# Optimization experiments

Measured on AMD Instinct MI355X. Metric: run time of the kernel, lower is better.

## Reference

```python
import jax, jax.numpy as jnp
import numpy as np

N = 50000      # nodes
E = 1600000    # edges (avg degree 32)
IN = 128       # input feature dim
H = 4          # heads
C = 16         # out channels per head
NEG_SLOPE = 0.2


def setup_inputs() -> dict:
    key = jax.random.key(0)
    k = jax.random.split(key, 6)
    x = jax.random.normal(k[0], (N, IN), jnp.float32)
    edge_index = jax.random.randint(k[1], (2, E), 0, N, dtype=jnp.int32).astype(jnp.int64)
    W = jax.random.normal(k[2], (H * C, IN), jnp.float32) * (1.0 / np.sqrt(IN))
    att_src = jax.random.normal(k[3], (H, C), jnp.float32) * 0.1
    att_dst = jax.random.normal(k[4], (H, C), jnp.float32) * 0.1
    bias = jax.random.normal(k[5], (H * C,), jnp.float32) * 0.01
    return {"x": x, "edge_index": edge_index, "W": W,
            "att_src": att_src, "att_dst": att_dst, "bias": bias}


def reference(x, edge_index, W, att_src, att_dst, bias):
    # shared linear projection (PyG GATConv lin, no bias): [N, H, C]
    xp = (x @ W.T).reshape(-1, H, C)
    # per-node attention logits: [N, H]
    a_src = jnp.einsum('nhc,hc->nh', xp, att_src)
    a_dst = jnp.einsum('nhc,hc->nh', xp, att_dst)
    src, dst = edge_index[0], edge_index[1]  # messages flow src(j) -> dst(i)
    # per-edge scores: [E, H]
    e = jax.nn.leaky_relu(a_src[src] + a_dst[dst], negative_slope=NEG_SLOPE)
    # segment softmax over destination neighborhoods
    m = jax.ops.segment_max(e, dst, num_segments=N)           # [N, H]
    m = jnp.where(jnp.isfinite(m), m, 0.0)                     # empty segments
    ex = jnp.exp(e - m[dst])
    s = jax.ops.segment_sum(ex, dst, num_segments=N)           # [N, H]
    alpha = ex / (s[dst] + 1e-16)                              # [E, H]
    # weighted messages, scatter-add to destinations
    msg = (alpha[:, :, None] * xp[src]).reshape(E, H * C)      # [E, H*C]
    out = jax.ops.segment_sum(msg, dst, num_segments=N)        # [N, H*C]
    return out + bias
```

## Files before the change

kernel.cpp:

```cpp
#include <hip/hip_runtime.h>
#include <hip/hip_bf16.h>
#include <math.h>

#define N_NODES 50000
#define N_EDGES 1600000
#define IN_DIM  128
#define HC      64
#define NH      4
#define SLOTS   72
#define BSHIFT  4
#define BNODES  16
#define NB      3125
#define BCAP    768
#define GEMM_BLOCKS 391
#define FAT_GRID 587
#define FAT_LDS 33792

__global__ __launch_bounds__(512) void gemm_bucket_kernel(
    const float* __restrict__ x, const float* __restrict__ W,
    const float* __restrict__ att_src, const float* __restrict__ att_dst,
    const int* __restrict__ ei,
    __hip_bfloat16* __restrict__ xp, float* __restrict__ a_src,
    float* __restrict__ a_dst,
    int* __restrict__ gcursor, unsigned int* __restrict__ barr) {
    extern __shared__ char smraw[];
    int tid = (int)threadIdx.x;
    int bx  = (int)blockIdx.x;
    bool is_bucket = (bx % 3) == 1;

    if (!is_bucket) {
        int gb = bx - (bx + 1) / 3;
        float* Wl = (float*)smraw;
        const float4* W4 = (const float4*)W;
#pragma unroll
        for (int j = 0; j < 4; ++j) {
            int f = j * 512 + tid;
            int c = f >> 5, k4 = f & 31;
            *(float4*)&Wl[c * 132 + k4 * 4] = W4[f];
        }
        __syncthreads();

        int l = tid & 63, w = tid >> 6, q = l >> 4, i = l & 15;
        int n0 = gb * 128 + w * 16 + q * 4;
        int nj[4];
#pragma unroll
        for (int j = 0; j < 4; ++j) {
            int n = n0 + j;
            nj[j] = (n < N_NODES) ? n : N_NODES - 1;
        }
        const float* wlp = Wl + i * 132;
        float4 acc[4] = {{0,0,0,0},{0,0,0,0},{0,0,0,0},{0,0,0,0}};
        float4 xr[4], xn[4];
#pragma unroll
        for (int j = 0; j < 4; ++j) xr[j] = *(const float4*)(x + (size_t)nj[j] * IN_DIM);
#pragma unroll 2
        for (int k0 = 0; k0 < IN_DIM; k0 += 4) {
            if (k0 + 4 < IN_DIM) {
#pragma unroll
                for (int j = 0; j < 4; ++j)
                    xn[j] = *(const float4*)(x + (size_t)nj[j] * IN_DIM + k0 + 4);
            }
            float4 wl0 = *(const float4*)(wlp + 0 * 16 * 132 + k0);
            float4 wl1 = *(const float4*)(wlp + 1 * 16 * 132 + k0);
            float4 wl2 = *(const float4*)(wlp + 2 * 16 * 132 + k0);
            float4 wl3 = *(const float4*)(wlp + 3 * 16 * 132 + k0);
#pragma unroll
            for (int j = 0; j < 4; ++j) {
                float4 xv = xr[j];
                acc[j].x = fmaf(xv.x, wl0.x, fmaf(xv.y, wl0.y, fmaf(xv.z, wl0.z, fmaf(xv.w, wl0.w, acc[j].x))));
                acc[j].y = fmaf(xv.x, wl1.x, fmaf(xv.y, wl1.y, fmaf(xv.z, wl1.z, fmaf(xv.w, wl1.w, acc[j].y))));
                acc[j].z = fmaf(xv.x, wl2.x, fmaf(xv.y, wl2.y, fmaf(xv.z, wl2.z, fmaf(xv.w, wl2.w, acc[j].z))));
                acc[j].w = fmaf(xv.x, wl3.x, fmaf(xv.y, wl3.y, fmaf(xv.z, wl3.z, fmaf(xv.w, wl3.w, acc[j].w))));
            }
#pragma unroll
            for (int j = 0; j < 4; ++j) xr[j] = xn[j];
        }

        float a_s0 = att_src[i], a_s1 = att_src[16 + i], a_s2 = att_src[32 + i], a_s3 = att_src[48 + i];
        float a_d0 = att_dst[i], a_d1 = att_dst[16 + i], a_d2 = att_dst[32 + i], a_d3 = att_dst[48 + i];
#pragma unroll
        for (int j = 0; j < 4; ++j) {
            int n = n0 + j;
            if (n < N_NODES) {
                __hip_bfloat16* xw = xp + (size_t)n * HC;
                xw[i]      = __float2bfloat16(acc[j].x);
                xw[16 + i] = __float2bfloat16(acc[j].y);
                xw[32 + i] = __float2bfloat16(acc[j].z);
                xw[48 + i] = __float2bfloat16(acc[j].w);
                float4 ps, pd;
                ps.x = acc[j].x * a_s0; ps.y = acc[j].y * a_s1;
                ps.z = acc[j].z * a_s2; ps.w = acc[j].w * a_s3;
                pd.x = acc[j].x * a_d0; pd.y = acc[j].y * a_d1;
                pd.z = acc[j].z * a_d2; pd.w = acc[j].w * a_d3;
#pragma unroll
                for (int off = 1; off < 16; off <<= 1) {
                    ps.x += __shfl_xor(ps.x, off, 64); ps.y += __shfl_xor(ps.y, off, 64);
                    ps.z += __shfl_xor(ps.z, off, 64); ps.w += __shfl_xor(ps.w, off, 64);
                    pd.x += __shfl_xor(pd.x, off, 64); pd.y += __shfl_xor(pd.y, off, 64);
                    pd.z += __shfl_xor(pd.z, off, 64); pd.w += __shfl_xor(pd.w, off, 64);
                }
                if (i == 0) {
                    *(float4*)(a_src + n * NH) = ps;
                    *(float4*)(a_dst + n * NH) = pd;
                }
            }
        }
    } else {
        int bb = (bx - 1) / 3;
        int* lcount = (int*)smraw;
        int* lbase  = lcount + NB;
        for (int j = tid; j < NB; j += 512) lcount[j] = 0;
        __syncthreads();
        int gid = bb * 512 + tid;
        bool active = gid < N_EDGES / 16;
        int s[16], d[16], b[16], lpos[16];
        if (active) {
            const int4* sp = (const int4*)ei;
            const int4* dp = (const int4*)(ei + N_EDGES);
#pragma unroll
            for (int v = 0; v < 4; ++v) {
                int4 sv = sp[4 * gid + v];
                int4 dv = dp[4 * gid + v];
                s[4*v+0] = sv.x; s[4*v+1] = sv.y; s[4*v+2] = sv.z; s[4*v+3] = sv.w;
                d[4*v+0] = dv.x; d[4*v+1] = dv.y; d[4*v+2] = dv.z; d[4*v+3] = dv.w;
            }
#pragma unroll
            for (int u = 0; u < 16; ++u) {
                b[u] = d[u] >> BSHIFT;
                lpos[u] = atomicAdd(&lcount[b[u]], 1);
            }
        }
        __syncthreads();
        for (int j = tid; j < NB; j += 512) {
            int c = lcount[j];
            lbase[j] = (c > 0) ? atomicAdd(&gcursor[j], c) : 0;
        }
        __syncthreads();
        if (active) {
#pragma unroll
            for (int u = 0; u < 16; ++u) {
                int pos = lbase[b[u]] + lpos[u];
                if (pos < BCAP)
                    barr[(size_t)b[u] * BCAP + pos] =
                        (unsigned)s[u] | ((unsigned)(d[u] & (BNODES - 1)) << 20);
            }
        }
    }
}

__global__ __launch_bounds__(128) void fused_gather_kernel(
    const unsigned int* __restrict__ barr, const int* __restrict__ gcursor,
    const float* __restrict__ a_src, const float* __restrict__ a_dst,
    const __hip_bfloat16* __restrict__ xp, const float* __restrict__ bias,
    float* __restrict__ out) {
    __shared__ int lcsr[BNODES * SLOTS];
    __shared__ int deg[BNODES];
    int b = blockIdx.x, tid = (int)threadIdx.x;
    if (tid < BNODES) deg[tid] = 0;
    __syncthreads();
    int n = gcursor[b];
    n = (n < BCAP) ? n : BCAP;
    const unsigned int* src = barr + (size_t)b * BCAP;

    for (int i0 = 0; i0 < n; i0 += 512) {
        int ibase = i0 + tid * 4;
        unsigned v[4]; bool val[4]; int dp[4], pos[4];
        if (ibase < n) {
            uint4 r = *(const uint4*)(src + ibase);
            v[0] = r.x; v[1] = r.y; v[2] = r.z; v[3] = r.w;
        } else { v[0] = v[1] = v[2] = v[3] = 0u; }
#pragma unroll
        for (int u = 0; u < 4; ++u) {
            val[u] = (ibase + u) < n;
            dp[u] = (int)(v[u] >> 20);
            if (val[u]) pos[u] = atomicAdd(&deg[dp[u]], 1);
        }
#pragma unroll
        for (int u = 0; u < 4; ++u)
            if (val[u] && pos[u] < SLOTS)
                lcsr[dp[u] * SLOTS + pos[u]] = (int)(v[u] & 0xFFFFF);
    }
    __syncthreads();

    int l = tid & 63;
    int w = tid >> 6;
    int g = l >> 3;
    int i = l & 7;
    int h = i >> 1;
    int dl = w * 8 + g;
    int dst = (b << BSHIFT) + dl;
    int dg = deg[dl];
    dg = (dg < SLOTS) ? dg : SLOTS;
    float adh = a_dst[dst * NH + h];

    int sreg[9];
#pragma unroll
    for (int k = 0; k < 9; ++k) sreg[k] = lcsr[dl * SLOTS + k * 8 + i];

    const unsigned short* xpi = (const unsigned short*)xp + 8 * i;
    const float* asrch = a_src + h;
    int gsel = l & 56;
    float a0=0,a1=0,a2=0,a3=0,a4=0,a5=0,a6=0,a7=0;
    float dsum = 0.f;

#pragma unroll
    for (int k = 0; k < 9; ++k) {
        if (dg > k * 8) {
            int cnt = dg - k * 8;
            int reg = sreg[k];
            int s8[8]; float g8[8]; uint4 t8[8];
#pragma unroll
            for (int u = 0; u < 8; ++u) {
                int raw = __shfl(reg, gsel | u, 64);
                s8[u] = (u < cnt) ? raw : 0;
            }
#pragma unroll
            for (int u = 0; u < 8; ++u) g8[u] = asrch[s8[u] * NH];
#pragma unroll
            for (int u = 0; u < 8; ++u)
                t8[u] = *(const uint4*)(xpi + (size_t)s8[u] * HC);
#pragma unroll
            for (int u = 0; u < 8; ++u) {
                float e = g8[u] + adh;
                e = fmaxf(e, 0.2f * e);
                float wv = (u < cnt) ? __expf(e) : 0.f;
                dsum += wv;
                uint4 t = t8[u];
                a0 = fmaf(wv, __uint_as_float(t.x << 16),          a0);
                a1 = fmaf(wv, __uint_as_float(t.x & 0xffff0000u),  a1);
                a2 = fmaf(wv, __uint_as_float(t.y << 16),          a2);
                a3 = fmaf(wv, __uint_as_float(t.y & 0xffff0000u),  a3);
                a4 = fmaf(wv, __uint_as_float(t.z << 16),          a4);
                a5 = fmaf(wv, __uint_as_float(t.z & 0xffff0000u),  a5);
                a6 = fmaf(wv, __uint_as_float(t.w << 16),          a6);
                a7 = fmaf(wv, __uint_as_float(t.w & 0xffff0000u),  a7);
            }
        }
    }
    if (dst < N_NODES) {
        float inv = 1.f / (dsum + 1e-16f);
        float4 b0 = *(const float4*)(bias + 8 * i);
        float4 b1 = *(const float4*)(bias + 8 * i + 4);
        float4 o0, o1;
        o0.x = a0 * inv + b0.x; o0.y = a1 * inv + b0.y;
        o0.z = a2 * inv + b0.z; o0.w = a3 * inv + b0.w;
        o1.x = a4 * inv + b1.x; o1.y = a5 * inv + b1.y;
        o1.z = a6 * inv + b1.z; o1.w = a7 * inv + b1.w;
        float* op = out + (size_t)dst * HC + 8 * i;
        *(float4*)op = o0;
        *(float4*)(op + 4) = o1;
    }
}

extern "C" void kernel_launch(void* const* d_in, const int* in_sizes, int n_in,
                              void* d_out, int out_size, void* d_ws, size_t ws_size,
                              hipStream_t stream) {
    const float* x       = (const float*)d_in[0];
    const int*   ei      = (const int*)d_in[1];
    const float* W       = (const float*)d_in[2];
    const float* att_src = (const float*)d_in[3];
    const float* att_dst = (const float*)d_in[4];
    const float* bias    = (const float*)d_in[5];
    float* out = (float*)d_out;

    char* ws = (char*)d_ws;
    __hip_bfloat16* xp      = (__hip_bfloat16*)(ws);
    float*          a_srcv  = (float*)(ws + 6400000);
    float*          a_dstv  = (float*)(ws + 7200000);
    int*            gcursor = (int*)  (ws + 8000000);
    unsigned int*   barr    = (unsigned int*)(ws + 8012512);

    hipMemsetAsync(gcursor, 0, NB * sizeof(int), stream);
    gemm_bucket_kernel<<<FAT_GRID, 512, FAT_LDS, stream>>>(
        x, W, att_src, att_dst, ei, xp, a_srcv, a_dstv, gcursor, barr);
    fused_gather_kernel<<<NB, 128, 0, stream>>>(barr, gcursor,
                                                a_srcv, a_dstv, xp, bias, out);
}
```

Measured before the change: 147.7 us.

## Enlarge destination buckets to 64 nodes and give every block a bucketing share

Destination buckets grow from 16 to 64 nodes, so there are fewer, larger buckets and the gather kernel runs with 512 threads per block over 782 blocks. The fat kernel no longer splits blocks into GEMM and bucket roles. Every block now bins a contiguous slice of edges, and the first 391 blocks then also run the projection GEMM. This balances the work and cuts contention on the global atomic cursors. In exchange, edge loads become scalar instead of int4, the GEMM blocks carry extra serial work, and the larger bucket capacity raises the risk of overflow from skewed degree.

Measured after the change: 159.9 us. 1.08x slower.

```diff
diff --git a/kernel.cpp b/kernel.cpp
--- a/kernel.cpp
+++ b/kernel.cpp
@@ -8,10 +8,11 @@
 #define HC      64
 #define NH      4
 #define SLOTS   72
-#define BSHIFT  4
-#define BNODES  16
-#define NB      3125
-#define BCAP    768
+#define BSHIFT  6
+#define BNODES  64
+#define NB      782
+#define BCAP    2432
+#define EPB     2736
 #define GEMM_BLOCKS 391
 #define FAT_GRID 587
 #define FAT_LDS 33792
@@ -26,10 +27,44 @@
     extern __shared__ char smraw[];
     int tid = (int)threadIdx.x;
     int bx  = (int)blockIdx.x;
-    bool is_bucket = (bx % 3) == 1;
-
-    if (!is_bucket) {
-        int gb = bx - (bx + 1) / 3;
+
+    {
+        int* lcount = (int*)smraw;
+        int* lbase  = lcount + NB;
+        for (int j = tid; j < NB; j += 512) lcount[j] = 0;
+        __syncthreads();
+        int s[6], d[6], bk[6], lpos[6]; bool val[6];
+#pragma unroll
+        for (int u = 0; u < 6; ++u) {
+            int off = u * 512 + tid;
+            int e   = bx * EPB + off;
+            val[u]  = (off < EPB) && (e < N_EDGES);
+            int ee  = val[u] ? e : 0;
+            s[u] = ei[ee];
+            d[u] = ei[N_EDGES + ee];
+            bk[u] = d[u] >> BSHIFT;
+            if (val[u]) lpos[u] = atomicAdd(&lcount[bk[u]], 1);
+        }
+        __syncthreads();
+        for (int j = tid; j < NB; j += 512) {
+            int c = lcount[j];
+            lbase[j] = (c > 0) ? atomicAdd(&gcursor[j], c) : 0;
+        }
+        __syncthreads();
+#pragma unroll
+        for (int u = 0; u < 6; ++u) {
+            if (val[u]) {
+                int pos = lbase[bk[u]] + lpos[u];
+                if (pos < BCAP)
+                    barr[(size_t)bk[u] * BCAP + pos] =
+                        (unsigned)s[u] | ((unsigned)(d[u] & (BNODES - 1)) << 20);
+            }
+        }
+    }
+
+    if (bx < GEMM_BLOCKS) {
+        __syncthreads();
+        int gb = bx;
         float* Wl = (float*)smraw;
         const float4* W4 = (const float4*)W;
 #pragma unroll
@@ -105,50 +140,10 @@
                 }
             }
         }
-    } else {
-        int bb = (bx - 1) / 3;
-        int* lcount = (int*)smraw;
-        int* lbase  = lcount + NB;
-        for (int j = tid; j < NB; j += 512) lcount[j] = 0;
-        __syncthreads();
-        int gid = bb * 512 + tid;
-        bool active = gid < N_EDGES / 16;
-        int s[16], d[16], b[16], lpos[16];
-        if (active) {
-            const int4* sp = (const int4*)ei;
-            const int4* dp = (const int4*)(ei + N_EDGES);
-#pragma unroll
-            for (int v = 0; v < 4; ++v) {
-                int4 sv = sp[4 * gid + v];
-                int4 dv = dp[4 * gid + v];
-                s[4*v+0] = sv.x; s[4*v+1] = sv.y; s[4*v+2] = sv.z; s[4*v+3] = sv.w;
-                d[4*v+0] = dv.x; d[4*v+1] = dv.y; d[4*v+2] = dv.z; d[4*v+3] = dv.w;
-            }
-#pragma unroll
-            for (int u = 0; u < 16; ++u) {
-                b[u] = d[u] >> BSHIFT;
-                lpos[u] = atomicAdd(&lcount[b[u]], 1);
-            }
-        }
-        __syncthreads();
-        for (int j = tid; j < NB; j += 512) {
-            int c = lcount[j];
-            lbase[j] = (c > 0) ? atomicAdd(&gcursor[j], c) : 0;
-        }
-        __syncthreads();
-        if (active) {
-#pragma unroll
-            for (int u = 0; u < 16; ++u) {
-                int pos = lbase[b[u]] + lpos[u];
-                if (pos < BCAP)
-                    barr[(size_t)b[u] * BCAP + pos] =
-                        (unsigned)s[u] | ((unsigned)(d[u] & (BNODES - 1)) << 20);
-            }
-        }
     }
 }
 
-__global__ __launch_bounds__(128) void fused_gather_kernel(
+__global__ __launch_bounds__(512) void fused_gather_kernel(
     const unsigned int* __restrict__ barr, const int* __restrict__ gcursor,
     const float* __restrict__ a_src, const float* __restrict__ a_dst,
     const __hip_bfloat16* __restrict__ xp, const float* __restrict__ bias,
@@ -162,7 +157,7 @@
     n = (n < BCAP) ? n : BCAP;
     const unsigned int* src = barr + (size_t)b * BCAP;
 
-    for (int i0 = 0; i0 < n; i0 += 512) {
+    for (int i0 = 0; i0 < n; i0 += 2048) {
         int ibase = i0 + tid * 4;
         unsigned v[4]; bool val[4]; int dp[4], pos[4];
         if (ibase < n) {
@@ -191,7 +186,8 @@
     int dst = (b << BSHIFT) + dl;
     int dg = deg[dl];
     dg = (dg < SLOTS) ? dg : SLOTS;
-    float adh = a_dst[dst * NH + h];
+    int dstc = (dst < N_NODES) ? dst : 0;
+    float adh = a_dst[dstc * NH + h];
 
     int sreg[9];
 #pragma unroll
@@ -268,11 +264,11 @@
     float*          a_srcv  = (float*)(ws + 6400000);
     float*          a_dstv  = (float*)(ws + 7200000);
     int*            gcursor = (int*)  (ws + 8000000);
-    unsigned int*   barr    = (unsigned int*)(ws + 8012512);
+    unsigned int*   barr    = (unsigned int*)(ws + 8016384);
 
     hipMemsetAsync(gcursor, 0, NB * sizeof(int), stream);
     gemm_bucket_kernel<<<FAT_GRID, 512, FAT_LDS, stream>>>(
         x, W, att_src, att_dst, ei, xp, a_srcv, a_dstv, gcursor, barr);
-    fused_gather_kernel<<<NB, 128, 0, stream>>>(barr, gcursor,
+    fused_gather_kernel<<<NB, 512, 0, stream>>>(barr, gcursor,
                                                 a_srcv, a_dstv, xp, bias, out);
 }
```
